# Kernel tuning notes

Measured on AMD Instinct MI355X. Metric: run time of the kernel, lower is better.

## Reference

```python
import jax, jax.numpy as jnp
import numpy as np

EPS = 1e-12  # F.normalize default eps


def setup_inputs() -> dict:
    key = jax.random.key(0)
    k1, k2, k3, k4 = jax.random.split(key, 4)
    b, c, h, w = 4, 64, 256, 256
    n_class, n = 19, 20
    nc1 = n_class + 1
    content = jax.random.normal(k1, (b, c, h, w), dtype=jnp.float32)
    seg = jax.random.randint(k2, (b, h, w), 0, n_class, dtype=jnp.int32)
    # xavier-normal-ish init for memory params
    key_mem = jax.random.normal(k3, (nc1, c, n), dtype=jnp.float32) * np.sqrt(2.0 / (c + n))
    val_mem = jax.random.normal(k4, (nc1, n, c), dtype=jnp.float32) * np.sqrt(2.0 / (n + c))
    return {"content": content, "seg": seg, "key_mem": key_mem, "val_mem": val_mem}


def reference(content, seg, key_mem, val_mem):
    # content: [b,c,h,w]; seg: [b,h,w] int; key_mem: [K,c,n]; val_mem: [K,n,c], K=n_class+1
    b, c, h, w = content.shape
    K, _, n = key_mem.shape
    p = h * w
    # one-hot class routing (seg shifted by +1 as in original)
    onehot = jax.nn.one_hot(seg.reshape(b, p) + 1, K, dtype=content.dtype)  # [b,p,K]
    # L2-normalize content rows (masked rows in the original are either this
    # normalized vector, for the matching class, or exactly zero)
    cn = content.transpose(0, 2, 3, 1).reshape(b, p, c)
    cn = cn / jnp.maximum(jnp.linalg.norm(cn, axis=-1, keepdims=True), EPS)
    # L2-normalize keys over channel dim (dim=1 of [K,c,n])
    kn = key_mem / jnp.maximum(jnp.linalg.norm(key_mem, axis=1, keepdims=True), EPS)
    # scores for the matching class; non-matching rows are zero -> softmax = uniform 1/n
    scores = jnp.einsum('bpc,kcn->bkpn', cn, kn)         # [b,K,p,n]
    attn = jax.nn.softmax(scores, axis=-1)
    mask = onehot.transpose(0, 2, 1)[..., None]           # [b,K,p,1]
    weight = jnp.where(mask > 0, attn, 1.0 / n)           # [b,K,p,n]
    # bmm with values, then sum over class dim (fused into the einsum)
    out = jnp.einsum('bkpn,knc->bpc', weight, val_mem)    # [b,p,c]
    return out.reshape(b, h, w, c).transpose(0, 3, 1, 2)  # [b,c,h,w]
```

## Files before the change

kernel.cpp:

```cpp
#include <hip/hip_runtime.h>

typedef _Float16 h2 __attribute__((ext_vector_type(2)));
typedef _Float16 h8 __attribute__((ext_vector_type(8)));
typedef float f4 __attribute__((ext_vector_type(4)));
typedef unsigned int uint32;

#define NVAL 20
#define CDIM 64
#define HW   65536
#define NPIX (4*HW)

#define BLK   512
#define NWAVE (BLK/64)
#define MAXSUB  52
#define MAXSLOT (MAXSUB*16)

#define KN_OFF      0
#define KN_KSTRIDE  2560
#define VAL_OFF     (20*KN_KSTRIDE)
#define VAL_KSTRIDE 4096
#define VAL_CSTRIDE 64

#define ROW_STRIDE 144
#define ROWS_BYTES (BLK*ROW_STRIDE)
#define INV_OFF   ROWS_BYTES
#define PERM_OFF  (INV_OFF + BLK*4)
#define SCLS_OFF  (PERM_OFF + MAXSLOT*2)
#define CNT_OFF   (SCLS_OFF + MAXSUB*4)
#define BASE_OFF  (CNT_OFF + 24*4)
#define NT_OFF    (BASE_OFF + 24*4)
#define LDS_TOTAL (NT_OFF + 16)

static __device__ __forceinline__ h2 bch2(uint32 u) { return __builtin_bit_cast(h2, u); }
static __device__ __forceinline__ uint32 bcu(h2 v) { return __builtin_bit_cast(uint32, v); }
static __device__ __forceinline__ h8 bch8(uint4 u) { return __builtin_bit_cast(h8, u); }
static __device__ __forceinline__ h2 pkrtz(float a, float b) {
    return __builtin_bit_cast(h2, __builtin_amdgcn_cvt_pkrtz(a, b));
}

__global__ void prep_kernel(const float* __restrict__ key,
                            const float* __restrict__ val,
                            unsigned char* __restrict__ ws) {
    int i = blockIdx.x * 256 + threadIdx.x;
    if (i < 20*CDIM) {
        int k = i >> 6, c = i & 63;
        const float* vb = val + k*NVAL*CDIM + c;
        float v[NVAL];
        float s = 0.f;
        #pragma unroll
        for (int j = 0; j < NVAL; j++) { v[j] = vb[j*CDIM]; s += v[j]; }
        float t = 0.f;
        for (int kk = 0; kk < 20; kk++) {
            const float* vb2 = val + kk*NVAL*CDIM + c;
            #pragma unroll
            for (int j = 0; j < NVAL; j++) t += vb2[j*CDIM];
        }
        float rest = (t - s) * (1.0f/NVAL);
        uint32* row = (uint32*)(ws + VAL_OFF + (size_t)k*VAL_KSTRIDE + c*VAL_CSTRIDE);
        #pragma unroll
        for (int jp = 0; jp < 10; jp++) row[jp] = bcu(pkrtz(v[2*jp], v[2*jp+1]));
        row[10] = bcu(pkrtz(rest, 0.f));
        #pragma unroll
        for (int jp = 11; jp < 16; jp++) row[jp] = 0u;
    } else if (i < 20*CDIM + 20*NVAL) {
        int idx = i - 20*CDIM;
        int k = idx / NVAL, j = idx % NVAL;
        const float* kb = key + k*CDIM*NVAL + j;
        float x[CDIM];
        float ssq = 0.f;
        #pragma unroll
        for (int c = 0; c < CDIM; c++) { x[c] = kb[c*NVAL]; ssq = fmaf(x[c], x[c], ssq); }
        float inv = 1.0f / fmaxf(sqrtf(ssq), 1e-12f);
        uint32* row = (uint32*)(ws + KN_OFF + (size_t)k*KN_KSTRIDE + j*128);
        #pragma unroll
        for (int cp = 0; cp < 32; cp++) row[cp] = bcu(pkrtz(x[2*cp]*inv, x[2*cp+1]*inv));
    }
}

__global__ __launch_bounds__(BLK, 4) void main_kernel(
        const float* __restrict__ content, const int* __restrict__ seg,
        const unsigned char* __restrict__ tabs, float* __restrict__ out) {
    extern __shared__ unsigned char lds[];
    float* invA = (float*)(lds + INV_OFF);
    unsigned short* perm = (unsigned short*)(lds + PERM_OFF);
    int* scls = (int*)(lds + SCLS_OFF);
    int* cnt  = (int*)(lds + CNT_OFF);
    int* base = (int*)(lds + BASE_OFF);
    int* ntp  = (int*)(lds + NT_OFF);

    const int tid  = threadIdx.x;
    const int gp0  = blockIdx.x * BLK;
    const int b    = gp0 >> 16;
    const int pim0 = gp0 & (HW - 1);

    if (tid < 24) cnt[tid] = 0;
    if (tid < MAXSUB) scls[tid] = 0;
    for (int i = tid; i < MAXSLOT; i += BLK) perm[i] = 0xFFFFu;
    __syncthreads();

    const int cls = seg[gp0 + tid] + 1;
    const int myrank = atomicAdd(&cnt[cls], 1);

    {
        const float* cptr = content + (size_t)b * CDIM * HW + pim0 + tid;
        uint2* myrow = (uint2*)(lds + tid * ROW_STRIDE);
        float ssq = 0.f;
        #pragma unroll
        for (int q = 0; q < 16; q++) {
            float f0 = cptr[(size_t)(4*q+0) * HW];
            float f1 = cptr[(size_t)(4*q+1) * HW];
            float f2 = cptr[(size_t)(4*q+2) * HW];
            float f3 = cptr[(size_t)(4*q+3) * HW];
            ssq = fmaf(f0,f0,ssq); ssq = fmaf(f1,f1,ssq);
            ssq = fmaf(f2,f2,ssq); ssq = fmaf(f3,f3,ssq);
            uint2 o; o.x = bcu(pkrtz(f0,f1)); o.y = bcu(pkrtz(f2,f3));
            myrow[q] = o;
        }
        invA[tid] = 1.0f / fmaxf(sqrtf(ssq), 1e-12f);
    }
    __syncthreads();

    if (tid == 0) {
        int off = 0;
        for (int k = 1; k <= 20; k++) { base[k] = off; off += (cnt[k] + 15) & ~15; }
        *ntp = off >> 4;
    }
    __syncthreads();
    {
        int slot = base[cls] + myrank;
        perm[slot] = (unsigned short)tid;
        scls[slot >> 4] = cls;
    }
    __syncthreads();

    const int nsub = *ntp;
    const int ntw  = (nsub + 3) >> 2;
    const int wave = tid >> 6, lane = tid & 63;
    const int g = lane >> 4, r16 = lane & 15;

    for (int it = wave; it < ntw; it += NWAVE) {
        int uu[4], rowb[4];
        float invn[4];
        bool mine[4];
        #pragma unroll
        for (int n = 0; n < 4; n++) {
            int sN = it*4 + n;
            uu[n] = __builtin_amdgcn_readfirstlane(scls[sN]);
            int v = perm[sN*16 + r16];
            mine[n] = (v != 0xFFFF);
            int l = mine[n] ? v : 0;
            rowb[n] = l * ROW_STRIDE;
            invn[n] = invA[l];
        }

        f4 sacc[2][4];
        #pragma unroll
        for (int m = 0; m < 2; m++)
            #pragma unroll
            for (int n = 0; n < 4; n++) sacc[m][n] = (f4){0.f,0.f,0.f,0.f};
        #pragma unroll
        for (int n = 0; n < 4; n++) {
            const unsigned char* knc = tabs + KN_OFF + (size_t)uu[n] * KN_KSTRIDE;
            uint4 b0 = *(const uint4*)(lds + rowb[n] + (g*8)*2);
            uint4 b1 = *(const uint4*)(lds + rowb[n] + (32 + g*8)*2);
            #pragma unroll
            for (int m = 0; m < 2; m++) {
                uint4 a0 = *(const uint4*)(knc + (m*16 + r16)*128 + (g*8)*2);
                uint4 a1 = *(const uint4*)(knc + (m*16 + r16)*128 + (32 + g*8)*2);
                sacc[m][n] = __builtin_amdgcn_mfma_f32_16x16x32_f16(
                    bch8(a0), bch8(b0), sacc[m][n], 0, 0, 0);
                sacc[m][n] = __builtin_amdgcn_mfma_f32_16x16x32_f16(
                    bch8(a1), bch8(b1), sacc[m][n], 0, 0, 0);
            }
        }

        uint2 w0[4], w1[4];
        #pragma unroll
        for (int n = 0; n < 4; n++) {
            float e0[4], e1[4];
            #pragma unroll
            for (int r = 0; r < 4; r++) e0[r] = __expf(sacc[0][n][r] * invn[n]);
            float arg1 = (g == 0) ? invn[n] : 0.0f;
            #pragma unroll
            for (int r = 0; r < 4; r++) e1[r] = __expf(sacc[1][n][r] * arg1);
            float s = e0[0]+e0[1]+e0[2]+e0[3];
            s += (g == 0) ? (e1[0]+e1[1]+e1[2]+e1[3]) : 0.0f;
            s += __shfl_xor(s, 16, 64);
            s += __shfl_xor(s, 32, 64);
            float wsc = 1.0f / s;
            w0[n].x = bcu(pkrtz(e0[0]*wsc, e0[1]*wsc));
            w0[n].y = bcu(pkrtz(e0[2]*wsc, e0[3]*wsc));
            uint2 t1;
            if (g == 0)      { t1.x = bcu(pkrtz(e1[0]*wsc, e1[1]*wsc));
                               t1.y = bcu(pkrtz(e1[2]*wsc, e1[3]*wsc)); }
            else if (g == 1) { t1.x = 0x00003C00u; t1.y = 0u; }
            else             { t1.x = 0u; t1.y = 0u; }
            w1[n] = t1;
        }
        #pragma unroll
        for (int n = 0; n < 4; n++) {
            if (mine[n]) {
                *(uint2*)(lds + rowb[n] + g*8)      = w0[n];
                *(uint2*)(lds + rowb[n] + 32 + g*8) = w1[n];
            }
        }

        uint4 b_pv[4];
        #pragma unroll
        for (int n = 0; n < 4; n++)
            b_pv[n] = *(const uint4*)(lds + rowb[n] + g*16);
        #pragma unroll
        for (int n = 0; n < 4; n++) {
            const unsigned char* vc = tabs + VAL_OFF + (size_t)uu[n] * VAL_KSTRIDE;
            #pragma unroll
            for (int m = 0; m < 4; m++) {
                uint4 a = *(const uint4*)(vc + (m*16 + r16)*VAL_CSTRIDE + g*16);
                f4 o = (f4){0.f,0.f,0.f,0.f};
                o = __builtin_amdgcn_mfma_f32_16x16x32_f16(bch8(a), bch8(b_pv[n]), o, 0, 0, 0);
                uint2 ov; ov.x = bcu(pkrtz(o[0], o[1])); ov.y = bcu(pkrtz(o[2], o[3]));
                if (mine[n])
                    *(uint2*)(lds + rowb[n] + m*32 + g*8) = ov;
            }
        }
    }
    __syncthreads();

    {
        const uint2* r2 = (const uint2*)(lds + tid * ROW_STRIDE);
        float* obase = out + (size_t)b * CDIM * HW + pim0 + tid;
        #pragma unroll
        for (int q = 0; q < 16; q++) {
            uint2 v = r2[q];
            h2 x = bch2(v.x), y = bch2(v.y);
            obase[(size_t)(4*q+0) * HW] = (float)x[0];
            obase[(size_t)(4*q+1) * HW] = (float)x[1];
            obase[(size_t)(4*q+2) * HW] = (float)y[0];
            obase[(size_t)(4*q+3) * HW] = (float)y[1];
        }
    }
}

extern "C" void kernel_launch(void* const* d_in, const int* in_sizes, int n_in,
                              void* d_out, int out_size, void* d_ws, size_t ws_size,
                              hipStream_t stream) {
    const float* content = (const float*)d_in[0];
    const int*   seg     = (const int*)d_in[1];
    const float* key     = (const float*)d_in[2];
    const float* val     = (const float*)d_in[3];
    float* out = (float*)d_out;
    unsigned char* ws = (unsigned char*)d_ws;

    prep_kernel<<<7, 256, 0, stream>>>(key, val, ws);

    (void)hipFuncSetAttribute((const void*)main_kernel,
                              hipFuncAttributeMaxDynamicSharedMemorySize, LDS_TOTAL);
    main_kernel<<<NPIX/BLK, BLK, LDS_TOTAL, stream>>>(content, seg, ws, out);
}
```

Measured before the change: 47.96 us.

## Halve block size, pre-normalize rows in LDS, batch MFMA operand loads

Result: slower. 50.53 us (+5.4%).

```diff
diff --git a/kernel.cpp b/kernel.cpp
--- a/kernel.cpp
+++ b/kernel.cpp
@@ -10,9 +10,9 @@
 #define HW   65536
 #define NPIX (4*HW)
 
-#define BLK   512
+#define BLK   256
 #define NWAVE (BLK/64)
-#define MAXSUB  52
+#define MAXSUB  36
 #define MAXSLOT (MAXSUB*16)
 
 #define KN_OFF      0
@@ -23,8 +23,7 @@
 
 #define ROW_STRIDE 144
 #define ROWS_BYTES (BLK*ROW_STRIDE)
-#define INV_OFF   ROWS_BYTES
-#define PERM_OFF  (INV_OFF + BLK*4)
+#define PERM_OFF  ROWS_BYTES
 #define SCLS_OFF  (PERM_OFF + MAXSLOT*2)
 #define CNT_OFF   (SCLS_OFF + MAXSUB*4)
 #define BASE_OFF  (CNT_OFF + 24*4)
@@ -81,7 +80,6 @@
         const float* __restrict__ content, const int* __restrict__ seg,
         const unsigned char* __restrict__ tabs, float* __restrict__ out) {
     extern __shared__ unsigned char lds[];
-    float* invA = (float*)(lds + INV_OFF);
     unsigned short* perm = (unsigned short*)(lds + PERM_OFF);
     int* scls = (int*)(lds + SCLS_OFF);
     int* cnt  = (int*)(lds + CNT_OFF);
@@ -103,20 +101,22 @@
 
     {
         const float* cptr = content + (size_t)b * CDIM * HW + pim0 + tid;
+        float x[CDIM];
+        float ssq = 0.f;
+        #pragma unroll
+        for (int c = 0; c < CDIM; c++) {
+            x[c] = cptr[(size_t)c * HW];
+            ssq = fmaf(x[c], x[c], ssq);
+        }
+        float inv = 1.0f / fmaxf(sqrtf(ssq), 1e-12f);
         uint2* myrow = (uint2*)(lds + tid * ROW_STRIDE);
-        float ssq = 0.f;
         #pragma unroll
         for (int q = 0; q < 16; q++) {
-            float f0 = cptr[(size_t)(4*q+0) * HW];
-            float f1 = cptr[(size_t)(4*q+1) * HW];
-            float f2 = cptr[(size_t)(4*q+2) * HW];
-            float f3 = cptr[(size_t)(4*q+3) * HW];
-            ssq = fmaf(f0,f0,ssq); ssq = fmaf(f1,f1,ssq);
-            ssq = fmaf(f2,f2,ssq); ssq = fmaf(f3,f3,ssq);
-            uint2 o; o.x = bcu(pkrtz(f0,f1)); o.y = bcu(pkrtz(f2,f3));
+            uint2 o;
+            o.x = bcu(pkrtz(x[4*q+0]*inv, x[4*q+1]*inv));
+            o.y = bcu(pkrtz(x[4*q+2]*inv, x[4*q+3]*inv));
             myrow[q] = o;
         }
-        invA[tid] = 1.0f / fmaxf(sqrtf(ssq), 1e-12f);
     }
     __syncthreads();
 
@@ -128,7 +128,7 @@
     __syncthreads();
     {
         int slot = base[cls] + myrank;
-        perm[slot] = (unsigned short)tid;
+        perm[slot] = (unsigned short)(tid * ROW_STRIDE);
         scls[slot >> 4] = cls;
     }
     __syncthreads();
@@ -140,7 +140,6 @@
 
     for (int it = wave; it < ntw; it += NWAVE) {
         int uu[4], rowb[4];
-        float invn[4];
         bool mine[4];
         #pragma unroll
         for (int n = 0; n < 4; n++) {
@@ -148,39 +147,39 @@
             uu[n] = __builtin_amdgcn_readfirstlane(scls[sN]);
             int v = perm[sN*16 + r16];
             mine[n] = (v != 0xFFFF);
-            int l = mine[n] ? v : 0;
-            rowb[n] = l * ROW_STRIDE;
-            invn[n] = invA[l];
+            rowb[n] = mine[n] ? v : 0;
         }
 
         f4 sacc[2][4];
+        uint4 a0[2][4], a1[2][4], bx0[4], bx1[4];
+        #pragma unroll
+        for (int n = 0; n < 4; n++) {
+            const unsigned char* knc = tabs + KN_OFF + (size_t)uu[n] * KN_KSTRIDE;
+            bx0[n] = *(const uint4*)(lds + rowb[n] + g*16);
+            bx1[n] = *(const uint4*)(lds + rowb[n] + 64 + g*16);
+            #pragma unroll
+            for (int m = 0; m < 2; m++) {
+                a0[m][n] = *(const uint4*)(knc + (m*16 + r16)*128 + g*16);
+                a1[m][n] = *(const uint4*)(knc + (m*16 + r16)*128 + 64 + g*16);
+            }
+        }
         #pragma unroll
         for (int m = 0; m < 2; m++)
             #pragma unroll
-            for (int n = 0; n < 4; n++) sacc[m][n] = (f4){0.f,0.f,0.f,0.f};
-        #pragma unroll
-        for (int n = 0; n < 4; n++) {
-            const unsigned char* knc = tabs + KN_OFF + (size_t)uu[n] * KN_KSTRIDE;
-            uint4 b0 = *(const uint4*)(lds + rowb[n] + (g*8)*2);
-            uint4 b1 = *(const uint4*)(lds + rowb[n] + (32 + g*8)*2);
-            #pragma unroll
-            for (int m = 0; m < 2; m++) {
-                uint4 a0 = *(const uint4*)(knc + (m*16 + r16)*128 + (g*8)*2);
-                uint4 a1 = *(const uint4*)(knc + (m*16 + r16)*128 + (32 + g*8)*2);
-                sacc[m][n] = __builtin_amdgcn_mfma_f32_16x16x32_f16(
-                    bch8(a0), bch8(b0), sacc[m][n], 0, 0, 0);
-                sacc[m][n] = __builtin_amdgcn_mfma_f32_16x16x32_f16(
-                    bch8(a1), bch8(b1), sacc[m][n], 0, 0, 0);
-            }
-        }
+            for (int n = 0; n < 4; n++) {
+                f4 acc = (f4){0.f,0.f,0.f,0.f};
+                acc = __builtin_amdgcn_mfma_f32_16x16x32_f16(bch8(a0[m][n]), bch8(bx0[n]), acc, 0, 0, 0);
+                acc = __builtin_amdgcn_mfma_f32_16x16x32_f16(bch8(a1[m][n]), bch8(bx1[n]), acc, 0, 0, 0);
+                sacc[m][n] = acc;
+            }
 
         uint2 w0[4], w1[4];
         #pragma unroll
         for (int n = 0; n < 4; n++) {
             float e0[4], e1[4];
             #pragma unroll
-            for (int r = 0; r < 4; r++) e0[r] = __expf(sacc[0][n][r] * invn[n]);
-            float arg1 = (g == 0) ? invn[n] : 0.0f;
+            for (int r = 0; r < 4; r++) e0[r] = __expf(sacc[0][n][r]);
+            float arg1 = (g == 0) ? 1.0f : 0.0f;
             #pragma unroll
             for (int r = 0; r < 4; r++) e1[r] = __expf(sacc[1][n][r] * arg1);
             float s = e0[0]+e0[1]+e0[2]+e0[3];
```
